# Optimization experiments

Measured on AMD Instinct MI355X. Metric: run time of the kernel, lower is better.

The kernel has to match this reference:

```python
import jax, jax.numpy as jnp
import numpy as np

EMBED_DIM = 1024
NUM_HEADS = 16
HEAD_DIM = EMBED_DIM // NUM_HEADS
SCALING = HEAD_DIM ** -0.5


def setup_inputs() -> dict:
    key = jax.random.key(0)
    ks = jax.random.split(key, 11)
    B, S, E = 4, 2048, EMBED_DIM
    s = 1.0 / np.sqrt(E)
    return {
        "query": jax.random.normal(ks[0], (B, S, E), jnp.float32),
        "key": jax.random.normal(ks[1], (B, S, E), jnp.float32),
        "value": jax.random.normal(ks[2], (B, S, E), jnp.float32),
        "q_w": jax.random.normal(ks[3], (E, E), jnp.float32) * s,
        "q_b": jax.random.normal(ks[4], (E,), jnp.float32) * 0.01,
        "k_w": jax.random.normal(ks[5], (E, E), jnp.float32) * s,
        "k_b": jax.random.normal(ks[6], (E,), jnp.float32) * 0.01,
        "v_w": jax.random.normal(ks[7], (E, E), jnp.float32) * s,
        "v_b": jax.random.normal(ks[8], (E,), jnp.float32) * 0.01,
        "out_w": jax.random.normal(ks[9], (E, E), jnp.float32) * s,
        "out_b": jax.random.normal(ks[10], (E,), jnp.float32) * 0.01,
    }


def reference(query, key, value, q_w, q_b, k_w, k_b, v_w, v_b, out_w, out_b):
    B, S, E = query.shape
    H, D = NUM_HEADS, HEAD_DIM
    # torch Linear: x @ W.T + b
    q = (query @ q_w.T + q_b).reshape(B, S, H, D).transpose(0, 2, 1, 3)  # [B,H,S,D]
    k = (key @ k_w.T + k_b).reshape(B, -1, H, D).transpose(0, 2, 1, 3)
    v = (value @ v_w.T + v_b).reshape(B, -1, H, D).transpose(0, 2, 1, 3)
    attn_scores = jnp.einsum("bhsd,bhtd->bhst", q, k) * SCALING  # [B,H,S,S]
    attn_weights = jax.nn.softmax(attn_scores, axis=-1)
    attn_output = jnp.einsum("bhst,bhtd->bhsd", attn_weights, v)
    attn_output = attn_output.transpose(0, 2, 1, 3).reshape(B, S, E)
    return attn_output @ out_w.T + out_b
```

## Files before the change

### kernel.cpp

```cpp
#include <hip/hip_runtime.h>
#include <stdint.h>
#include <stddef.h>

#define BB 4
#define SS 2048
#define EE 1024
#define HH 16
#define DD 64
#define MTOT (BB * SS)

#define SOFTMAX_C (0.125f * 1.44269504088896340736f)

using bf16x8 = __attribute__((ext_vector_type(8))) __bf16;
using f32x4  = __attribute__((ext_vector_type(4))) float;
using s16x4  = __attribute__((ext_vector_type(4))) short;

__device__ inline unsigned short f2bf(float f) {
    union { float f; uint32_t u; } v; v.f = f;
    uint32_t u = v.u;
    u += 0x7fffu + ((u >> 16) & 1u);
    return (unsigned short)(u >> 16);
}

__device__ inline uint32_t packbf_trunc(float lo, float hi) {
    union { float f; uint32_t u; } a, b; a.f = lo; b.f = hi;
    return (a.u >> 16) | (b.u & 0xFFFF0000u);
}

__device__ inline void gld_lds16(const unsigned short* g, unsigned short* l) {
    __builtin_amdgcn_global_load_lds(
        (const __attribute__((address_space(1))) unsigned int*)g,
        (__attribute__((address_space(3))) unsigned int*)l,
        16, 0, 0);
}

__global__ __launch_bounds__(256) void cast3_f32_bf16(
    const float* __restrict__ a, const float* __restrict__ b,
    const float* __restrict__ c,
    unsigned short* __restrict__ oa, unsigned short* __restrict__ ob,
    unsigned short* __restrict__ oc, int n4) {
    int i = blockIdx.x * 256 + threadIdx.x;
    const float* src = (blockIdx.y == 0) ? a : (blockIdx.y == 1) ? b : c;
    unsigned short* dst = (blockIdx.y == 0) ? oa : (blockIdx.y == 1) ? ob : oc;
    if (i < n4) {
        float4 f = ((const float4*)src)[i];
        ushort4 o;
        o.x = f2bf(f.x); o.y = f2bf(f.y); o.z = f2bf(f.z); o.w = f2bf(f.w);
        ((ushort4*)dst)[i] = o;
    }
}

__global__ __launch_bounds__(256) void cast4_f32_bf16(
    const float* __restrict__ a, const float* __restrict__ b,
    const float* __restrict__ c, const float* __restrict__ d,
    unsigned short* __restrict__ oa, unsigned short* __restrict__ ob,
    unsigned short* __restrict__ oc, unsigned short* __restrict__ od, int n4) {
    int i = blockIdx.x * 256 + threadIdx.x;
    const float* src = (blockIdx.y == 0) ? a : (blockIdx.y == 1) ? b
                     : (blockIdx.y == 2) ? c : d;
    unsigned short* dst = (blockIdx.y == 0) ? oa : (blockIdx.y == 1) ? ob
                        : (blockIdx.y == 2) ? oc : od;
    if (i < n4) {
        float4 f = ((const float4*)src)[i];
        ushort4 o;
        o.x = f2bf(f.x); o.y = f2bf(f.y); o.z = f2bf(f.z); o.w = f2bf(f.w);
        ((ushort4*)dst)[i] = o;
    }
}

template <int MODE>
__global__ __launch_bounds__(256) void gemm_nt(
    const unsigned short* __restrict__ A,
    const unsigned short* __restrict__ W,
    const float* __restrict__ bias,
    void* __restrict__ outp, float oscale) {
    __shared__ __align__(16) unsigned short As[128 * 64];
    __shared__ __align__(16) unsigned short Bs[128 * 64];

    const int tid  = threadIdx.x;
    const int lane = tid & 63;
    const int wid  = tid >> 6;
    const int wm   = wid >> 1;
    const int wn   = wid & 1;
    const int quad = lane >> 4;
    const int l16  = lane & 15;
    const int m0   = blockIdx.y * 128;
    const int n0   = blockIdx.x * 128;

    f32x4 acc[4][4];
#pragma unroll
    for (int i = 0; i < 4; i++)
#pragma unroll
        for (int j = 0; j < 4; j++) acc[i][j] = (f32x4){0.f, 0.f, 0.f, 0.f};

    const int lrow = lane >> 3;
    const int lcol = (lane & 7) * 8;
    const unsigned short* ga = A + (size_t)(m0 + wid * 32 + lrow) * 1024 + lcol;
    const unsigned short* gb = W + (size_t)(n0 + wid * 32 + lrow) * 1024 + lcol;
    unsigned short* la = As + wid * 32 * 64;
    unsigned short* lb = Bs + wid * 32 * 64;

    for (int k0 = 0; k0 < 1024; k0 += 64) {
        __syncthreads();
#pragma unroll
        for (int c = 0; c < 4; c++) {
            gld_lds16(ga + (size_t)c * 8 * 1024 + k0, la + c * 8 * 64);
            gld_lds16(gb + (size_t)c * 8 * 1024 + k0, lb + c * 8 * 64);
        }
        __syncthreads();

#pragma unroll
        for (int kt = 0; kt < 2; kt++) {
            bf16x8 a[4], b[4];
#pragma unroll
            for (int mt = 0; mt < 4; mt++)
                a[mt] = *(const bf16x8*)(As + (wm * 64 + mt * 16 + l16) * 64 + kt * 32 + quad * 8);
#pragma unroll
            for (int nt = 0; nt < 4; nt++)
                b[nt] = *(const bf16x8*)(Bs + (wn * 64 + nt * 16 + l16) * 64 + kt * 32 + quad * 8);
#pragma unroll
            for (int mt = 0; mt < 4; mt++)
#pragma unroll
                for (int nt = 0; nt < 4; nt++)
                    acc[mt][nt] = __builtin_amdgcn_mfma_f32_16x16x32_bf16(
                        a[mt], b[nt], acc[mt][nt], 0, 0, 0);
        }
    }

#pragma unroll
    for (int mt = 0; mt < 4; mt++) {
#pragma unroll
        for (int nt = 0; nt < 4; nt++) {
            int gcol = n0 + wn * 64 + nt * 16 + l16;
            float bvn = (MODE != 3) ? bias[gcol] : 0.f;
#pragma unroll
            for (int r = 0; r < 4; r++) {
                int grow = m0 + wm * 64 + mt * 16 + quad * 4 + r;
                float bv = (MODE == 3) ? bias[grow] : bvn;
                float v = (acc[mt][nt][r] + bv) * oscale;
                if (MODE == 0) {
                    int bb = grow >> 11, sr = grow & 2047;
                    int hh = gcol >> 6,  dd = gcol & 63;
                    ((unsigned short*)outp)[(((size_t)(bb * HH + hh)) * SS + sr) * DD + dd] = f2bf(v);
                } else if (MODE == 3) {
                    int bb = gcol >> 11, sr = gcol & 2047;
                    int hh = grow >> 6,  dd = grow & 63;
                    ((unsigned short*)outp)[(((size_t)(bb * HH + hh)) * DD + dd) * SS + sr] = f2bf(v);
                } else {
                    ((float*)outp)[(size_t)grow * 1024 + gcol] = v;
                }
            }
        }
    }
}

__global__ __launch_bounds__(256) void flash_attn6(
    const unsigned short* __restrict__ Qh,
    const unsigned short* __restrict__ Kh,
    const unsigned short* __restrict__ Vtg,
    unsigned short* __restrict__ attn) {
    constexpr int LSK = 72;
    constexpr int LSV = 76;
    constexpr int BUFSZ = 64 * LSK + 64 * LSV;
    constexpr int NT = SS / 64;
    __shared__ __align__(16) unsigned short Sh[2 * BUFSZ];

    const int tid  = threadIdx.x;
    const int lane = tid & 63;
    const int w    = tid >> 6;
    const int quad = lane >> 4;
    const int l16  = lane & 15;
    const int bh   = blockIdx.y;
    const int q0   = blockIdx.x * 128;
    const size_t base = (size_t)bh * SS * DD;

    union { unsigned short u[4]; s16x4 v; } onesu;
#pragma unroll
    for (int i = 0; i < 4; i++) onesu.u[i] = 0x3F80;
    const s16x4 ones = onesu.v;

    bf16x8 bq[2][2];
#pragma unroll
    for (int s = 0; s < 2; s++)
#pragma unroll
        for (int kt = 0; kt < 2; kt++)
            bq[s][kt] = *(const bf16x8*)(Qh + base +
                (size_t)(q0 + w * 32 + s * 16 + l16) * DD + kt * 32 + quad * 8);

    f32x4 oT[2][4];
    f32x4 lacc[2];
#pragma unroll
    for (int s = 0; s < 2; s++) {
        lacc[s] = (f32x4){0.f, 0.f, 0.f, 0.f};
#pragma unroll
        for (int dt = 0; dt < 4; dt++) oT[s][dt] = (f32x4){0.f, 0.f, 0.f, 0.f};
    }

    const int crow = tid >> 3;
    const int ccol = (tid & 7) * 8;
    uint4 kreg[2], vreg[2];

    auto LOADT = [&](int j0) {
#pragma unroll
        for (int i = 0; i < 2; ++i) {
            kreg[i] = *(const uint4*)(Kh + base + (size_t)(j0 + crow + 32 * i) * DD + ccol);
            vreg[i] = *(const uint4*)(Vtg + base + (size_t)(crow + 32 * i) * SS + j0 + ccol);
        }
    };
    auto STORET = [&](unsigned short* KsD, unsigned short* VsD) {
#pragma unroll
        for (int i = 0; i < 2; ++i) {
            int row = crow + 32 * i;
            *(uint4*)(KsD + row * LSK + ccol) = kreg[i];
            *(uint2*)(VsD + row * LSV + ccol)     = uint2{vreg[i].x, vreg[i].y};
            *(uint2*)(VsD + row * LSV + ccol + 4) = uint2{vreg[i].z, vreg[i].w};
        }
    };

    auto COMPUTE = [&](const unsigned short* Ks, const unsigned short* Vs) {
        f32x4 sacc[2][4];
#pragma unroll
        for (int s = 0; s < 2; s++)
#pragma unroll
            for (int mt = 0; mt < 4; mt++) sacc[s][mt] = (f32x4){0.f, 0.f, 0.f, 0.f};
        __builtin_amdgcn_s_setprio(1);
#pragma unroll
        for (int kt = 0; kt < 2; kt++) {
            bf16x8 ak[4];
#pragma unroll
            for (int mt = 0; mt < 4; mt++)
                ak[mt] = *(const bf16x8*)(Ks + (mt * 16 + l16) * LSK + kt * 32 + quad * 8);
#pragma unroll
            for (int s = 0; s < 2; s++)
#pragma unroll
                for (int mt = 0; mt < 4; mt++)
                    sacc[s][mt] = __builtin_amdgcn_mfma_f32_16x16x32_bf16(
                        ak[mt], bq[s][kt], sacc[s][mt], 0, 0, 0);
        }
        __builtin_amdgcn_s_setprio(0);

        s16x4 bpf[2][4];
#pragma unroll
        for (int s = 0; s < 2; s++) {
#pragma unroll
            for (int mt = 0; mt < 4; mt++) {
                float p0 = __builtin_amdgcn_exp2f(sacc[s][mt][0]);
                float p1 = __builtin_amdgcn_exp2f(sacc[s][mt][1]);
                float p2 = __builtin_amdgcn_exp2f(sacc[s][mt][2]);
                float p3 = __builtin_amdgcn_exp2f(sacc[s][mt][3]);
                union { uint32_t w[2]; s16x4 v; } pk;
                pk.w[0] = packbf_trunc(p0, p1);
                pk.w[1] = packbf_trunc(p2, p3);
                bpf[s][mt] = pk.v;
                lacc[s] = __builtin_amdgcn_mfma_f32_16x16x16bf16_1k(
                    ones, pk.v, lacc[s], 0, 0, 0);
            }
        }

        __builtin_amdgcn_s_setprio(1);
#pragma unroll
        for (int mt = 0; mt < 4; mt++) {
#pragma unroll
            for (int dt = 0; dt < 4; dt++) {
                s16x4 av = *(const s16x4*)(Vs + (dt * 16 + l16) * LSV + mt * 16 + quad * 4);
#pragma unroll
                for (int s = 0; s < 2; s++)
                    oT[s][dt] = __builtin_amdgcn_mfma_f32_16x16x16bf16_1k(
                        av, bpf[s][mt], oT[s][dt], 0, 0, 0);
            }
        }
        __builtin_amdgcn_s_setprio(0);
    };

    LOADT(0);
    STORET(Sh, Sh + 64 * LSK);
    __syncthreads();

    for (int jt = 0; jt < NT - 1; ++jt) {
        const int cur = jt & 1;
        const unsigned short* Ks = Sh + cur * BUFSZ;
        LOADT((jt + 1) * 64);
        COMPUTE(Ks, Ks + 64 * LSK);
        unsigned short* Kn = Sh + (cur ^ 1) * BUFSZ;
        STORET(Kn, Kn + 64 * LSK);
        __syncthreads();
    }
    {
        const unsigned short* Ks = Sh + ((NT - 1) & 1) * BUFSZ;
        COMPUTE(Ks, Ks + 64 * LSK);
    }

    float inv_l[2];
#pragma unroll
    for (int s = 0; s < 2; s++) inv_l[s] = 1.f / lacc[s][0];

    __syncthreads();
#pragma unroll
    for (int s = 0; s < 2; s++)
#pragma unroll
        for (int dt = 0; dt < 4; dt++)
#pragma unroll
            for (int r = 0; r < 4; r++)
                Sh[(w * 32 + s * 16 + l16) * LSK + dt * 16 + quad * 4 + r] =
                    f2bf(oT[s][dt][r] * inv_l[s]);
    __syncthreads();

    const int b = bh >> 4, h = bh & 15;
#pragma unroll
    for (int i = 0; i < 4; i++) {
        int c = tid + 256 * i;
        int row = c >> 3, col8 = (c & 7) * 8;
        *(uint4*)(attn + ((size_t)b * SS + q0 + row) * EE + h * 64 + col8) =
            *(const uint4*)(Sh + row * LSK + col8);
    }
}

extern "C" void kernel_launch(void* const* d_in, const int* in_sizes, int n_in,
                              void* d_out, int out_size, void* d_ws, size_t ws_size,
                              hipStream_t stream) {
    (void)in_sizes; (void)n_in; (void)out_size; (void)ws_size;
    const float* q_in  = (const float*)d_in[0];
    const float* k_in  = (const float*)d_in[1];
    const float* v_in  = (const float*)d_in[2];
    const float* q_w   = (const float*)d_in[3];
    const float* q_b   = (const float*)d_in[4];
    const float* k_w   = (const float*)d_in[5];
    const float* k_b   = (const float*)d_in[6];
    const float* v_w   = (const float*)d_in[7];
    const float* v_b   = (const float*)d_in[8];
    const float* out_w = (const float*)d_in[9];
    const float* out_b = (const float*)d_in[10];

    const size_t NX = (size_t)MTOT * EE;
    const size_t NW = (size_t)EE * EE;

    unsigned short* xq = (unsigned short*)d_ws;
    unsigned short* xk = xq + NX;
    unsigned short* xv = xk + NX;
    unsigned short* wq = xv + NX;
    unsigned short* wk = wq + NW;
    unsigned short* wv = wk + NW;
    unsigned short* wo = wv + NW;
    unsigned short* qh = wo + NW;
    unsigned short* kh = qh + NX;
    unsigned short* vt = kh + NX;
    unsigned short* attn = vt + NX;

    cast3_f32_bf16<<<dim3((int)(NX / 4 / 256), 3), 256, 0, stream>>>(
        q_in, k_in, v_in, xq, xk, xv, (int)(NX / 4));
    cast4_f32_bf16<<<dim3((int)(NW / 4 / 256), 4), 256, 0, stream>>>(
        q_w, k_w, v_w, out_w, wq, wk, wv, wo, (int)(NW / 4));

    dim3 ggrid(EE / 128, MTOT / 128);
    dim3 ggridT(MTOT / 128, EE / 128);
    gemm_nt<0><<<ggrid, 256, 0, stream>>>(xq, wq, q_b, qh, SOFTMAX_C);
    gemm_nt<0><<<ggrid, 256, 0, stream>>>(xk, wk, k_b, kh, 1.0f);
    gemm_nt<3><<<ggridT, 256, 0, stream>>>(wv, xv, v_b, vt, 1.0f);

    flash_attn6<<<dim3(SS / 128, BB * HH), 256, 0, stream>>>(qh, kh, vt, attn);

    gemm_nt<1><<<ggrid, 256, 0, stream>>>(attn, wo, out_b, (float*)d_out, 1.0f);
}
```

Before: 396.6 us.

## Double-buffer GEMM LDS tiles and stage bf16 epilogue through shared memory

The projection GEMM now double-buffers its K tiles in a single 64KB LDS array, issuing the next tile's global-to-LDS loads before computing the current one, and uses one barrier per iteration instead of two. The bf16 output modes write results into LDS first and then emit coalesced 16-byte stores, rather than scattered 2-byte stores. The Q/K projection now writes row-major [B,S,E] output, and the attention kernel reads Q and K with a strided head offset. Doubling LDS use may lower occupancy, and the strided Q/K reads may reduce locality in the attention kernel.

After: 383.5 us. 1.03x faster.

```diff
diff --git a/kernel.cpp b/kernel.cpp
--- a/kernel.cpp
+++ b/kernel.cpp
@@ -74,8 +74,7 @@
     const unsigned short* __restrict__ W,
     const float* __restrict__ bias,
     void* __restrict__ outp, float oscale) {
-    __shared__ __align__(16) unsigned short As[128 * 64];
-    __shared__ __align__(16) unsigned short Bs[128 * 64];
+    __shared__ __align__(16) unsigned short Smem[32768];
 
     const int tid  = threadIdx.x;
     const int lane = tid & 63;
@@ -97,18 +96,25 @@
     const int lcol = (lane & 7) * 8;
     const unsigned short* ga = A + (size_t)(m0 + wid * 32 + lrow) * 1024 + lcol;
     const unsigned short* gb = W + (size_t)(n0 + wid * 32 + lrow) * 1024 + lcol;
-    unsigned short* la = As + wid * 32 * 64;
-    unsigned short* lb = Bs + wid * 32 * 64;
-
-    for (int k0 = 0; k0 < 1024; k0 += 64) {
-        __syncthreads();
+
+    auto STAGE = [&](int buf, int k0) {
+        unsigned short* la = Smem + buf * 16384 + wid * 32 * 64;
+        unsigned short* lb = la + 8192;
 #pragma unroll
         for (int c = 0; c < 4; c++) {
             gld_lds16(ga + (size_t)c * 8 * 1024 + k0, la + c * 8 * 64);
             gld_lds16(gb + (size_t)c * 8 * 1024 + k0, lb + c * 8 * 64);
         }
-        __syncthreads();
-
+    };
+
+    STAGE(0, 0);
+    __syncthreads();
+
+    for (int t = 0; t < 16; ++t) {
+        const int cur = t & 1;
+        if (t < 15) STAGE(cur ^ 1, (t + 1) * 64);
+        const unsigned short* As = Smem + cur * 16384;
+        const unsigned short* Bs = As + 8192;
 #pragma unroll
         for (int kt = 0; kt < 2; kt++) {
             bf16x8 a[4], b[4];
@@ -125,32 +131,59 @@
                     acc[mt][nt] = __builtin_amdgcn_mfma_f32_16x16x32_bf16(
                         a[mt], b[nt], acc[mt][nt], 0, 0, 0);
         }
-    }
-
-#pragma unroll
-    for (int mt = 0; mt < 4; mt++) {
-#pragma unroll
-        for (int nt = 0; nt < 4; nt++) {
-            int gcol = n0 + wn * 64 + nt * 16 + l16;
-            float bvn = (MODE != 3) ? bias[gcol] : 0.f;
-#pragma unroll
-            for (int r = 0; r < 4; r++) {
-                int grow = m0 + wm * 64 + mt * 16 + quad * 4 + r;
-                float bv = (MODE == 3) ? bias[grow] : bvn;
-                float v = (acc[mt][nt][r] + bv) * oscale;
-                if (MODE == 0) {
-                    int bb = grow >> 11, sr = grow & 2047;
-                    int hh = gcol >> 6,  dd = gcol & 63;
-                    ((unsigned short*)outp)[(((size_t)(bb * HH + hh)) * SS + sr) * DD + dd] = f2bf(v);
-                } else if (MODE == 3) {
-                    int bb = gcol >> 11, sr = gcol & 2047;
-                    int hh = grow >> 6,  dd = grow & 63;
-                    ((unsigned short*)outp)[(((size_t)(bb * HH + hh)) * DD + dd) * SS + sr] = f2bf(v);
-                } else {
-                    ((float*)outp)[(size_t)grow * 1024 + gcol] = v;
+        __syncthreads();
+    }
+
+    if (MODE == 0 || MODE == 3) {
+        constexpr int OS = 136;
+        unsigned short* Os = Smem;
+#pragma unroll
+        for (int mt = 0; mt < 4; mt++)
+#pragma unroll
+            for (int nt = 0; nt < 4; nt++) {
+                int cl = wn * 64 + nt * 16 + l16;
+                float bvn = (MODE == 0) ? bias[n0 + cl] : 0.f;
+#pragma unroll
+                for (int r = 0; r < 4; r++) {
+                    int rl = wm * 64 + mt * 16 + quad * 4 + r;
+                    float bv = (MODE == 3) ? bias[m0 + rl] : bvn;
+                    Os[rl * OS + cl] = f2bf((acc[mt][nt][r] + bv) * oscale);
                 }
             }
-        }
+        __syncthreads();
+        if (MODE == 0) {
+#pragma unroll
+            for (int i = 0; i < 8; i++) {
+                int c = tid + 256 * i;
+                int row = c >> 4, g = c & 15;
+                *(uint4*)((unsigned short*)outp + (size_t)(m0 + row) * 1024 + n0 + g * 8)
+                    = *(const uint4*)(Os + row * OS + g * 8);
+            }
+        } else {
+            const int bb = n0 >> 11, s0 = n0 & 2047;
+#pragma unroll
+            for (int i = 0; i < 8; i++) {
+                int c = tid + 256 * i;
+                int row = c >> 4, g = c & 15;
+                int hh = (m0 + row) >> 6, dd = (m0 + row) & 63;
+                *(uint4*)((unsigned short*)outp + (((size_t)(bb * HH + hh)) * DD + dd) * SS + s0 + g * 8)
+                    = *(const uint4*)(Os + row * OS + g * 8);
+            }
+        }
+    } else {
+#pragma unroll
+        for (int mt = 0; mt < 4; mt++)
+#pragma unroll
+            for (int nt = 0; nt < 4; nt++) {
+                int gcol = n0 + wn * 64 + nt * 16 + l16;
+                float bvn = bias[gcol];
+#pragma unroll
+                for (int r = 0; r < 4; r++) {
+                    int grow = m0 + wm * 64 + mt * 16 + quad * 4 + r;
+                    ((float*)outp)[(size_t)grow * 1024 + gcol] =
+                        (acc[mt][nt][r] + bvn) * oscale;
+                }
+            }
     }
 }
 
@@ -172,7 +205,9 @@
     const int l16  = lane & 15;
     const int bh   = blockIdx.y;
     const int q0   = blockIdx.x * 128;
-    const size_t base = (size_t)bh * SS * DD;
+    const int b    = bh >> 4, h = bh & 15;
+    const size_t baseqk = (size_t)b * SS * EE + h * 64;
+    const size_t basev  = (size_t)bh * SS * DD;
 
     union { unsigned short u[4]; s16x4 v; } onesu;
 #pragma unroll
@@ -184,8 +219,8 @@
     for (int s = 0; s < 2; s++)
 #pragma unroll
         for (int kt = 0; kt < 2; kt++)
-            bq[s][kt] = *(const bf16x8*)(Qh + base +
-                (size_t)(q0 + w * 32 + s * 16 + l16) * DD + kt * 32 + quad * 8);
+            bq[s][kt] = *(const bf16x8*)(Qh + baseqk +
+                (size_t)(q0 + w * 32 + s * 16 + l16) * EE + kt * 32 + quad * 8);
 
     f32x4 oT[2][4];
     f32x4 lacc[2];
@@ -203,8 +238,8 @@
     auto LOADT = [&](int j0) {
 #pragma unroll
         for (int i = 0; i < 2; ++i) {
-            kreg[i] = *(const uint4*)(Kh + base + (size_t)(j0 + crow + 32 * i) * DD + ccol);
-            vreg[i] = *(const uint4*)(Vtg + base + (size_t)(crow + 32 * i) * SS + j0 + ccol);
+            kreg[i] = *(const uint4*)(Kh + baseqk + (size_t)(j0 + crow + 32 * i) * EE + ccol);
+            vreg[i] = *(const uint4*)(Vtg + basev + (size_t)(crow + 32 * i) * SS + j0 + ccol);
         }
     };
     auto STORET = [&](unsigned short* KsD, unsigned short* VsD) {
@@ -305,7 +340,6 @@
                     f2bf(oT[s][dt][r] * inv_l[s]);
     __syncthreads();
 
-    const int b = bh >> 4, h = bh & 15;
 #pragma unroll
     for (int i = 0; i < 4; i++) {
         int c = tid + 256 * i;
```
